# Kernel tuning notes

Hardware: AMD Instinct MI355X
Metric: run time of the kernel (lower is better)

Reference implementation:

```python
import jax, jax.numpy as jnp
import numpy as np

TEMP = 0.5  # init kwarg `tmp`
NUM_CLASSES = 100


def setup_inputs() -> dict:
    key = jax.random.key(0)
    k1, k2 = jax.random.split(key)
    embedding = jax.random.normal(k1, (8192, 256), dtype=jnp.float32)
    label = jax.random.randint(k2, (8192,), 0, NUM_CLASSES, dtype=jnp.int64)
    return {"embedding": embedding, "label": label}


def reference(embedding, label):
    # Row-normalize -> pairwise cosine similarity [N, N]
    normed = embedding / jnp.linalg.norm(embedding, axis=1, keepdims=True)
    sim = (normed @ normed.T) / TEMP  # already divided by temperature

    N = embedding.shape[0]
    eye = jnp.eye(N, dtype=bool)

    # Denominator: sum of exp(sim) over off-diagonal entries per row
    exp_sim = jnp.exp(sim)
    row_sum = jnp.sum(jnp.where(eye, 0.0, exp_sim), axis=1)  # [N]

    # log(exp(sim_ij) / row_sum_i) = sim_ij - log(row_sum_i)
    log_prob = sim - jnp.log(row_sum)[:, None]

    # Positive mask: same label, i != j
    pos_mask = (label[:, None] == label[None, :]) & ~eye
    n_i = jnp.sum(pos_mask, axis=1)  # positives per anchor

    inner = jnp.sum(jnp.where(pos_mask, log_prob, 0.0), axis=1)  # [N]
    per_anchor = jnp.where(n_i > 0, -inner / jnp.maximum(n_i, 1).astype(sim.dtype), 0.0)
    return jnp.sum(per_anchor)
```

## Files before the change

### kernel.cpp

```cpp
#include <hip/hip_runtime.h>
#include <hip/hip_bf16.h>
#include <stdint.h>

#define N    8192
#define D    256
#define NCLS 100

static constexpr float TEMP    = 0.5f;
static constexpr float SCALE_F = 1.69864360f;
static constexpr float E2      = 7.38905609893065f;
static constexpr float LN2     = 0.69314718055994531f;

typedef float f32x4 __attribute__((ext_vector_type(4)));

__device__ __forceinline__ unsigned short f2bf(float f) {
  union { float f; unsigned int u; } x; x.f = f;
  unsigned int r = x.u + 0x7fffu + ((x.u >> 16) & 1u);
  return (unsigned short)(r >> 16);
}
__device__ __forceinline__ float bf2f(unsigned short b) {
  union { unsigned int u; float f; } x; x.u = ((unsigned int)b) << 16;
  return x.f;
}
__device__ __forceinline__ void gld16(const void* g, void* l) {
  __builtin_amdgcn_global_load_lds(
      (const __attribute__((address_space(1))) unsigned int*)g,
      (__attribute__((address_space(3))) unsigned int*)l, 16, 0, 0);
}


__global__ __launch_bounds__(256) void normalize_kernel(
    const float* __restrict__ emb, const long long* __restrict__ label,
    unsigned short* __restrict__ abf, unsigned char* __restrict__ a8,
    int* __restrict__ cnt, int* __restrict__ list) {
  const int row  = blockIdx.x * 4 + (threadIdx.x >> 6);
  const int lane = threadIdx.x & 63;
  const float4 v = ((const float4*)(emb + (size_t)row * D))[lane];
  float ss = v.x * v.x + v.y * v.y + v.z * v.z + v.w * v.w;
#pragma unroll
  for (int off = 1; off < 64; off <<= 1) ss += __shfl_xor(ss, off);
  const float s = rsqrtf(ss) * SCALE_F;
  const float x = v.x * s, y = v.y * s, z = v.z * s, wv = v.w * s;

  ushort4 o;
  o.x = f2bf(x); o.y = f2bf(y); o.z = f2bf(z); o.w = f2bf(wv);
  ((ushort4*)(abf + (size_t)row * D))[lane] = o;

  int p = __builtin_amdgcn_cvt_pk_fp8_f32(x, y, 0, false);
  p = __builtin_amdgcn_cvt_pk_fp8_f32(z, wv, p, true);
  *(int*)(a8 + (size_t)(row >> 4) * 4096 + (lane >> 1) * 128 +
          (row & 15) * 8 + (lane & 1) * 4) = p;

  if (lane == 0) {
    const int c = (int)label[row];
    const int slot = atomicAdd(cnt + c, 1);
    list[c * 256 + slot] = row;
  }
}

#define TM 128
#define TN 128
#define JT 4

__global__ __launch_bounds__(256) void simexp_rowsum_kernel(
    const unsigned char* __restrict__ A, float* __restrict__ rowsum) {
  __shared__ __align__(16) unsigned char sa[TM * 128];
  __shared__ __align__(16) unsigned char sb[TN * 128];
  const int tid  = threadIdx.x;
  const int w    = tid >> 6;
  const int lane = tid & 63;
  const int quad = lane >> 4;
  const int l15  = lane & 15;
  const int row0 = blockIdx.y * TM;
  const int jc0  = blockIdx.x * (TN * JT);
  const int pr0  = row0 >> 4;
  const int pam  = (w & 1) * 4;
  const int pbn  = (w >> 1) * 4;
  const int wm   = (w & 1) * 64;
  const int wn   = (w >> 1) * 64;

  float rowpart[4][4];
#pragma unroll
  for (int mt = 0; mt < 4; ++mt)
#pragma unroll
    for (int e = 0; e < 4; ++e) rowpart[mt][e] = 0.f;

  for (int jt = 0; jt < JT; ++jt) {
    const int jbase = jc0 + jt * TN;
    const int pj0   = jbase >> 4;
    f32x4 acc[4][4];
#pragma unroll
    for (int mt = 0; mt < 4; ++mt)
#pragma unroll
      for (int nt = 0; nt < 4; ++nt) acc[mt][nt] = (f32x4){0.f, 0.f, 0.f, 0.f};

#pragma unroll
    for (int kc = 0; kc < 2; ++kc) {
#pragma unroll
      for (int p = 0; p < 4; ++p) {
        const int seg  = p * 4 + w;
        const int pp   = seg >> 1;
        const int half = (seg & 1) * 1024;
        const size_t goff = kc * 2048 + half + lane * 16;
        gld16(A + (size_t)(pr0 + pp) * 4096 + goff, sa + seg * 1024);
        gld16(A + (size_t)(pj0 + pp) * 4096 + goff, sb + seg * 1024);
      }
      __syncthreads();
#pragma unroll
      for (int kk = 0; kk < 4; ++kk) {
        const int fo = (kk * 4 + quad) * 128 + l15 * 8;
        long af[4], bf[4];
#pragma unroll
        for (int mt = 0; mt < 4; ++mt)
          af[mt] = *(const long*)(sa + (pam + mt) * 2048 + fo);
#pragma unroll
        for (int nt = 0; nt < 4; ++nt)
          bf[nt] = *(const long*)(sb + (pbn + nt) * 2048 + fo);
#pragma unroll
        for (int mt = 0; mt < 4; ++mt)
#pragma unroll
          for (int nt = 0; nt < 4; ++nt)
            acc[mt][nt] = __builtin_amdgcn_mfma_f32_16x16x32_fp8_fp8(
                af[mt], bf[nt], acc[mt][nt], 0, 0, 0);
      }
      __syncthreads();
    }

#pragma unroll
    for (int mt = 0; mt < 4; ++mt)
#pragma unroll
      for (int nt = 0; nt < 4; ++nt)
#pragma unroll
        for (int e = 0; e < 4; ++e)
          rowpart[mt][e] += __builtin_amdgcn_exp2f(acc[mt][nt][e]);
  }

#pragma unroll
  for (int mt = 0; mt < 4; ++mt)
#pragma unroll
    for (int e = 0; e < 4; ++e) {
      float v = rowpart[mt][e];
      v += __shfl_xor(v, 1);
      v += __shfl_xor(v, 2);
      v += __shfl_xor(v, 4);
      v += __shfl_xor(v, 8);
      if (l15 == 0)
        atomicAdd(&rowsum[row0 + wm + mt * 16 + quad * 4 + e], v);
    }
  (void)wn;
}

__global__ __launch_bounds__(256) void finalize_kernel(
    const unsigned short* __restrict__ abf, const float* __restrict__ rowsum,
    const long long* __restrict__ label, const int* __restrict__ cnt,
    const int* __restrict__ list, float* __restrict__ out) {
  __shared__ float red[4];
  __shared__ int rows_l[256];
  const int tid  = threadIdx.x;
  const int w    = tid >> 6;
  const int lane = tid & 63;

  if (blockIdx.x < NCLS) {
    const int c = blockIdx.x;
    const int m = cnt[c];
    if (m <= 1) return;
    if (tid < m) rows_l[tid] = list[c * 256 + tid];
    __syncthreads();
    float acc = 0.f;
    for (int s = 0; s < m; ++s)
      acc += bf2f(abf[(size_t)rows_l[s] * D + tid]);
    float v = acc * acc;
#pragma unroll
    for (int off = 1; off < 64; off <<= 1) v += __shfl_xor(v, off);
    if (lane == 0) red[w] = v;
    __syncthreads();
    if (tid == 0) {
      const float ssq = red[0] + red[1] + red[2] + red[3];
      const float term = (ssq * LN2 - 2.0f * (float)m) / (float)(m - 1);
      atomicAdd(out, -term);
    }
  } else {
    const int i = (blockIdx.x - NCLS) * 256 + tid;
    const int c = (int)label[i];
    float v = 0.f;
    if (cnt[c] > 1)
      v = __builtin_amdgcn_logf(rowsum[i] - E2) * LN2;
#pragma unroll
    for (int off = 1; off < 64; off <<= 1) v += __shfl_xor(v, off);
    if (lane == 0) red[w] = v;
    __syncthreads();
    if (tid == 0)
      atomicAdd(out, red[0] + red[1] + red[2] + red[3]);
  }
}

extern "C" void kernel_launch(void* const* d_in, const int* in_sizes, int n_in,
                              void* d_out, int out_size, void* d_ws,
                              size_t ws_size, hipStream_t stream) {
  const float* emb = (const float*)d_in[0];
  const long long* label = (const long long*)d_in[1];
  float* out = (float*)d_out;

  char* ws = (char*)d_ws;
  unsigned short* abf = (unsigned short*)ws;
  unsigned char* a8 = (unsigned char*)(ws + (size_t)N * D * 2);
  float* rowsum = (float*)(ws + (size_t)N * D * 3);
  int* cnt = (int*)(rowsum + N);
  int* list = cnt + 128;

  hipMemsetAsync(rowsum, 0, (size_t)N * 4 + 128 * 4, stream);
  hipMemsetAsync(out, 0, sizeof(float), stream);

  normalize_kernel<<<N / 4, 256, 0, stream>>>(emb, label, abf, a8, cnt, list);

  dim3 gridB(N / (TN * JT), N / TM);
  simexp_rowsum_kernel<<<gridB, 256, 0, stream>>>(a8, rowsum);

  finalize_kernel<<<NCLS + N / 256, 256, 0, stream>>>(abf, rowsum, label, cnt,
                                                      list, out);
}
```

Baseline: 132.9 us.

## Keep full-K A tile resident and double-buffer B loads in simexp kernel

The similarity/exp kernel now loads the whole 128x256 FP8 A tile into shared memory once, instead of reloading it for every column tile and K chunk. B tiles are double-buffered, so the next chunk's global-to-LDS load is issued before the MFMA work on the current chunk, with one barrier per step. Rowsum zeroing moves into the normalize kernel, which shrinks the memset to just the class counters. The trade-off is that shared memory per block doubles to 64KB, which could limit occupancy, and correctness depends on the async LDS loads finishing before the barrier.

```diff
diff --git a/kernel.cpp b/kernel.cpp
--- a/kernel.cpp
+++ b/kernel.cpp
@@ -32,7 +32,8 @@
 __global__ __launch_bounds__(256) void normalize_kernel(
     const float* __restrict__ emb, const long long* __restrict__ label,
     unsigned short* __restrict__ abf, unsigned char* __restrict__ a8,
-    int* __restrict__ cnt, int* __restrict__ list) {
+    float* __restrict__ rowsum, int* __restrict__ cnt,
+    int* __restrict__ list) {
   const int row  = blockIdx.x * 4 + (threadIdx.x >> 6);
   const int lane = threadIdx.x & 63;
   const float4 v = ((const float4*)(emb + (size_t)row * D))[lane];
@@ -52,6 +53,7 @@
           (row & 15) * 8 + (lane & 1) * 4) = p;
 
   if (lane == 0) {
+    rowsum[row] = 0.f;
     const int c = (int)label[row];
     const int slot = atomicAdd(cnt + c, 1);
     list[c * 256 + slot] = row;
@@ -64,8 +66,8 @@
 
 __global__ __launch_bounds__(256) void simexp_rowsum_kernel(
     const unsigned char* __restrict__ A, float* __restrict__ rowsum) {
-  __shared__ __align__(16) unsigned char sa[TM * 128];
-  __shared__ __align__(16) unsigned char sb[TN * 128];
+  __shared__ __align__(16) unsigned char sa[TM * 256];
+  __shared__ __align__(16) unsigned char sb[2][TN * 128];
   const int tid  = threadIdx.x;
   const int w    = tid >> 6;
   const int lane = tid & 63;
@@ -77,7 +79,21 @@
   const int pam  = (w & 1) * 4;
   const int pbn  = (w >> 1) * 4;
   const int wm   = (w & 1) * 64;
-  const int wn   = (w >> 1) * 64;
+
+#pragma unroll
+  for (int p = 0; p < 8; ++p) {
+    const int seg = w * 8 + p;
+    gld16(A + (size_t)(pr0 + (seg >> 2)) * 4096 + (seg & 3) * 1024 + lane * 16,
+          sa + seg * 1024);
+  }
+#pragma unroll
+  for (int p = 0; p < 4; ++p) {
+    const int seg = w * 4 + p;
+    gld16(A + (size_t)((jc0 >> 4) + (seg >> 1)) * 4096 + (seg & 1) * 1024 +
+              lane * 16,
+          sb[0] + seg * 1024);
+  }
+  __syncthreads();
 
   float rowpart[4][4];
 #pragma unroll
@@ -85,9 +101,8 @@
 #pragma unroll
     for (int e = 0; e < 4; ++e) rowpart[mt][e] = 0.f;
 
+  int buf = 0;
   for (int jt = 0; jt < JT; ++jt) {
-    const int jbase = jc0 + jt * TN;
-    const int pj0   = jbase >> 4;
     f32x4 acc[4][4];
 #pragma unroll
     for (int mt = 0; mt < 4; ++mt)
@@ -96,26 +111,28 @@
 
 #pragma unroll
     for (int kc = 0; kc < 2; ++kc) {
-#pragma unroll
-      for (int p = 0; p < 4; ++p) {
-        const int seg  = p * 4 + w;
-        const int pp   = seg >> 1;
-        const int half = (seg & 1) * 1024;
-        const size_t goff = kc * 2048 + half + lane * 16;
-        gld16(A + (size_t)(pr0 + pp) * 4096 + goff, sa + seg * 1024);
-        gld16(A + (size_t)(pj0 + pp) * 4096 + goff, sb + seg * 1024);
+      if (!(jt == JT - 1 && kc == 1)) {
+        const int njt = (kc == 1) ? jt + 1 : jt;
+        const int nkc = kc ^ 1;
+        const int pj0 = (jc0 + njt * TN) >> 4;
+#pragma unroll
+        for (int p = 0; p < 4; ++p) {
+          const int seg = w * 4 + p;
+          gld16(A + (size_t)(pj0 + (seg >> 1)) * 4096 + nkc * 2048 +
+                    (seg & 1) * 1024 + lane * 16,
+                sb[buf ^ 1] + seg * 1024);
+        }
       }
-      __syncthreads();
 #pragma unroll
       for (int kk = 0; kk < 4; ++kk) {
         const int fo = (kk * 4 + quad) * 128 + l15 * 8;
         long af[4], bf[4];
 #pragma unroll
         for (int mt = 0; mt < 4; ++mt)
-          af[mt] = *(const long*)(sa + (pam + mt) * 2048 + fo);
+          af[mt] = *(const long*)(sa + (pam + mt) * 4096 + kc * 2048 + fo);
 #pragma unroll
         for (int nt = 0; nt < 4; ++nt)
-          bf[nt] = *(const long*)(sb + (pbn + nt) * 2048 + fo);
+          bf[nt] = *(const long*)(sb[buf] + (pbn + nt) * 2048 + fo);
 #pragma unroll
         for (int mt = 0; mt < 4; ++mt)
 #pragma unroll
@@ -124,6 +141,7 @@
                 af[mt], bf[nt], acc[mt][nt], 0, 0, 0);
       }
       __syncthreads();
+      buf ^= 1;
     }
 
 #pragma unroll
@@ -147,7 +165,6 @@
       if (l15 == 0)
         atomicAdd(&rowsum[row0 + wm + mt * 16 + quad * 4 + e], v);
     }
-  (void)wn;
 }
 
 __global__ __launch_bounds__(256) void finalize_kernel(
@@ -208,10 +225,11 @@
   int* cnt = (int*)(rowsum + N);
   int* list = cnt + 128;
 
-  hipMemsetAsync(rowsum, 0, (size_t)N * 4 + 128 * 4, stream);
+  hipMemsetAsync(cnt, 0, 128 * 4, stream);
   hipMemsetAsync(out, 0, sizeof(float), stream);
 
-  normalize_kernel<<<N / 4, 256, 0, stream>>>(emb, label, abf, a8, cnt, list);
+  normalize_kernel<<<N / 4, 256, 0, stream>>>(emb, label, abf, a8, rowsum,
+                                              cnt, list);
 
   dim3 gridB(N / (TN * JT), N / TM);
   simexp_rowsum_kernel<<<gridB, 256, 0, stream>>>(a8, rowsum);
```

New measurement: 132.3 us (median of 2 runs). About the same (-0.4%).
